# Performance work log

Measured on AMD Instinct MI355X. Metric: run time of the kernel, lower is better.

The kernel has to match this reference:

```python
import jax, jax.numpy as jnp
import numpy as np
import math

B, S, H, NH, DK, K = 256, 200, 768, 12, 64, 64
EPS = 1e-12

def setup_inputs() -> dict:
    key = jax.random.key(0)
    ks = jax.random.split(key, 8)
    sc = 0.02
    return {
        "x": jax.random.normal(ks[0], (B, S, H), dtype=jnp.float32),
        "mask": jnp.ones((B, 1, S), dtype=jnp.float32),
        "Wq": jax.random.normal(ks[1], (H, H), dtype=jnp.float32) * sc,
        "bq": jnp.zeros((H,), dtype=jnp.float32),
        "Wk": jax.random.normal(ks[2], (H, H), dtype=jnp.float32) * sc,
        "bk": jnp.zeros((H,), dtype=jnp.float32),
        "Wv": jax.random.normal(ks[3], (H, H), dtype=jnp.float32) * sc,
        "bv": jnp.zeros((H,), dtype=jnp.float32),
        "We": jax.random.normal(ks[4], (K, S), dtype=jnp.float32) * sc,
        "be": jnp.zeros((K,), dtype=jnp.float32),
        "Wf": jax.random.normal(ks[5], (K, S), dtype=jnp.float32) * sc,
        "bf": jnp.zeros((K,), dtype=jnp.float32),
        "Wd": jax.random.normal(ks[6], (H, H), dtype=jnp.float32) * sc,
        "bd": jnp.zeros((H,), dtype=jnp.float32),
        "gamma": jnp.ones((H,), dtype=jnp.float32),
        "beta": jnp.zeros((H,), dtype=jnp.float32),
    }

def _heads(t):  # [B,S,H] -> [B,NH,S,DK]
    return t.reshape(B, S, NH, DK).transpose(0, 2, 1, 3)

def reference(x, mask, Wq, bq, Wk, bk, Wv, bv, We, be, Wf, bf, Wd, bd, gamma, beta):
    q = _heads(x @ Wq.T + bq)
    k = _heads(x @ Wk.T + bk)
    v = _heads(x @ Wv.T + bv)
    m = mask[:, 0:1, :, None]            # [B,1,S,1]
    k = k * m
    v = v * m
    # Linformer seq projections: E on value, F on key (applied along seq axis)
    v = jnp.einsum("bhsd,ks->bhkd", v, We) + be[:, None]   # [B,NH,K,DK]
    k = jnp.einsum("bhsd,ks->bhkd", k, Wf) + bf[:, None]   # [B,NH,K,DK]
    scores = jnp.einsum("bhqd,bhkd->bhqk", q, k) / math.sqrt(DK)
    p_attn = jax.nn.softmax(scores, axis=-1)               # [B,NH,S,K]
    ctx = jnp.einsum("bhqk,bhkd->bhqd", p_attn, v)         # [B,NH,S,DK]
    ctx = ctx.transpose(0, 2, 1, 3).reshape(B, S, H)
    h = ctx @ Wd.T + bd + x                                # dense + residual (dropout=0)
    mu = jnp.mean(h, axis=-1, keepdims=True)
    var = jnp.mean(jnp.square(h - mu), axis=-1, keepdims=True)
    out = (h - mu) / jnp.sqrt(var + EPS) * gamma + beta
    return out, p_attn
```

## Files before the change

### kernel.cpp

```cpp
#include <hip/hip_runtime.h>
#include <stdint.h>

typedef unsigned short u16;
typedef short bf16x8 __attribute__((ext_vector_type(8)));
typedef float f32x4 __attribute__((ext_vector_type(4)));

#define NB   256
#define NS   200
#define NHID 768
#define NHEAD 12
#define NDK  64
#define NK   64
#define NBH  (NB*NHEAD)
#define NM   (NB*NS)
#define SP   224

__device__ __forceinline__ u16 f2b(float f){
  unsigned u = __builtin_bit_cast(unsigned, f);
  return (u16)((u + 0x7FFFu + ((u>>16)&1u)) >> 16);
}
__device__ __forceinline__ bf16x8 pack8(const float* v){
  bf16x8 r;
#pragma unroll
  for (int i=0;i<8;i++) r[i] = (short)f2b(v[i]);
  return r;
}
__device__ __forceinline__ f32x4 mfma16(bf16x8 a, bf16x8 b, f32x4 c){
  return __builtin_amdgcn_mfma_f32_16x16x32_bf16(a, b, c, 0, 0, 0);
}
__device__ __forceinline__ void gload16(u16* l, const u16* g){
  __builtin_amdgcn_global_load_lds(
      (const __attribute__((address_space(1))) void*)g,
      (__attribute__((address_space(3))) void*)l, 16, 0, 0);
}

__global__ __launch_bounds__(256) void pack_w(
    const float* __restrict__ Wq, const float* __restrict__ Wk,
    const float* __restrict__ Wv, const float* __restrict__ Wd,
    u16* __restrict__ Wqb, u16* __restrict__ Wkb,
    u16* __restrict__ Wvb, u16* __restrict__ Wdb)
{
  const int i = blockIdx.x*256 + threadIdx.x;
  Wqb[i]=f2b(Wq[i]); Wkb[i]=f2b(Wk[i]); Wvb[i]=f2b(Wv[i]); Wdb[i]=f2b(Wd[i]);
}

__global__ __launch_bounds__(256) void pack_wfe(
    const float* __restrict__ Wf, const float* __restrict__ We, u16* __restrict__ Wfeb)
{
  const int r = blockIdx.x, s = threadIdx.x;
  if (s < SP){
    float v = 0.f;
    if (s < NS) v = (r<64) ? Wf[r*NS+s] : We[(r-64)*NS+s];
    Wfeb[r*SP+s] = f2b(v);
  }
}

__global__ __launch_bounds__(128) void rowsums_k(
    const float* __restrict__ Wf, const float* __restrict__ We,
    const float* __restrict__ mask, float* __restrict__ rs)
{
  const int b = blockIdx.x, kk = threadIdx.x;
  const float* src = (kk<64) ? (Wf + kk*NS) : (We + (kk-64)*NS);
  float acc = 0.f;
  for (int s=0;s<NS;s++) acc += src[s]*mask[b*NS+s];
  rs[b*128+kk] = acc;
}

__global__ __launch_bounds__(256) void transpose_x(
    const float* __restrict__ x, const float* __restrict__ mask,
    u16* __restrict__ xb, u16* __restrict__ xbT)
{
  __shared__ u16 LT[64*232];
  const int t = threadIdx.x, b = blockIdx.x, n0 = blockIdx.y*64;
  for (int i=0;i<50;i++){
    const int idx = i*256 + t;
    const int s = idx>>6, n = idx&63;
    const size_t gi = ((size_t)b*NS + s)*NHID + n0 + n;
    const float v = x[gi];
    xb[gi] = f2b(v);
    const float mv = mask[b*NS+s];
    LT[n*232 + s] = f2b(v*mv);
  }
  __syncthreads();
  const int row = t>>2, cb = t&3;
  u16* dst = xbT + (size_t)b*NHID*SP + (size_t)(n0+row)*SP;
  for (int i=0;i<7;i++){
    const int c = cb + i*4;
    bf16x8 vv = (c<25) ? *(const bf16x8*)&LT[row*232 + c*8] : (bf16x8)0;
    *(bf16x8*)&dst[c*8] = vv;
  }
}

__global__ __launch_bounds__(256) void gemm_yfe(
    const u16* __restrict__ Wfeb, const u16* __restrict__ xbT, u16* __restrict__ yfe)
{
  __shared__ u16 Al[128*64];
  __shared__ u16 Bl[128*64];
  const int t=threadIdx.x, w=t>>6, lane=t&63, hi=lane>>4, lo=lane&15;
  const int sr=lane>>3, sc=lane&7;
  const int b=blockIdx.x, col0=blockIdx.y*128;
  const u16* Bg = xbT + (size_t)b*NHID*SP;
  f32x4 acc[4][4];
#pragma unroll
  for(int i=0;i<4;i++)
#pragma unroll
    for(int j=0;j<4;j++) acc[i][j]=(f32x4)0.0f;
  const u16* Ab=&Al[((w>>1)*64+lo)*64 + hi*8];
  const u16* Bb=&Bl[((w&1)*64+lo)*64 + hi*8];

  for (int kt=0; kt<192; kt+=64){
#pragma unroll
    for (int i8=0;i8<4;i8++){
      const int r = w*32 + i8*8 + sr;
      gload16(&Al[r*64 + sc*8], Wfeb + (size_t)r*SP + kt + sc*8);
      gload16(&Bl[r*64 + sc*8], Bg + (size_t)(col0+r)*SP + kt + sc*8);
    }
    asm volatile("s_waitcnt vmcnt(0)" ::: "memory");
    __syncthreads();
#pragma unroll
    for (int ks=0; ks<2; ks++){
      bf16x8 a[4], bfr[4];
#pragma unroll
      for (int i=0;i<4;i++) a[i]   = *(const bf16x8*)(Ab + i*16*64 + ks*32);
#pragma unroll
      for (int j=0;j<4;j++) bfr[j] = *(const bf16x8*)(Bb + j*16*64 + ks*32);
#pragma unroll
      for (int i=0;i<4;i++)
#pragma unroll
        for (int j=0;j<4;j++) acc[i][j] = mfma16(a[i], bfr[j], acc[i][j]);
    }
    __syncthreads();
  }
#pragma unroll
  for (int i8=0;i8<2;i8++){
    const int r2 = w*32 + i8*16 + (lane>>2);
    gload16(&Al[r2*32 + (lane&3)*8], Wfeb + (size_t)r2*SP + 192 + (lane&3)*8);
    gload16(&Bl[r2*32 + (lane&3)*8], Bg + (size_t)(col0+r2)*SP + 192 + (lane&3)*8);
  }
  asm volatile("s_waitcnt vmcnt(0)" ::: "memory");
  __syncthreads();
  {
    bf16x8 a[4], bfr[4];
#pragma unroll
    for (int i=0;i<4;i++) a[i]   = *(const bf16x8*)&Al[((w>>1)*64+i*16+lo)*32 + hi*8];
#pragma unroll
    for (int j=0;j<4;j++) bfr[j] = *(const bf16x8*)&Bl[((w&1)*64+j*16+lo)*32 + hi*8];
#pragma unroll
    for (int i=0;i<4;i++)
#pragma unroll
      for (int j=0;j<4;j++) acc[i][j] = mfma16(a[i], bfr[j], acc[i][j]);
  }
  const int mbase=(w>>1)*64, nbase=col0+(w&1)*64;
#pragma unroll
  for (int i=0;i<4;i++)
#pragma unroll
    for (int r=0;r<4;r++){
      const int m = mbase + i*16 + hi*4 + r;
#pragma unroll
      for (int j=0;j<4;j++){
        const int n = nbase + j*16 + lo;
        yfe[(size_t)b*98304 + (size_t)m*NHID + n] = f2b(acc[i][j][r]);
      }
    }
}

template<int EPI>
__global__ __launch_bounds__(512, 2) void gemm_ring(
    const u16* __restrict__ Ag_, const u16* __restrict__ Bg_,
    const float* __restrict__ bias, const float* __restrict__ resid,
    void* __restrict__ Cout)
{
  __shared__ u16 AS[4][8192];
  __shared__ u16 BS[4][8192];
  const int t = threadIdx.x;
  const int w = t>>6, lane = t&63, hi = lane>>4, lo = lane&15;
  const int wm = w>>2, wn = w&3;
  const int row0 = blockIdx.x*256, col0 = blockIdx.y*256;
  const u16* Ag = Ag_ + (size_t)row0*NHID;
  const u16* Bg = Bg_ + (size_t)col0*NHID;
  const int rp0 = t>>3, cc = t&7;

  f32x4 acc[8][4];
#pragma unroll
  for (int i=0;i<8;i++)
#pragma unroll
    for (int j=0;j<4;j++) acc[i][j] = (f32x4)0.0f;

  int aoff[8], boff[4];
#pragma unroll
  for (int i=0;i<8;i++){
    const int r = wm*128 + i*16 + lo;
    const int rp = r>>1, c = (r&1)*4 + hi;
    aoff[i] = rp*64 + ((c ^ (rp&7))<<3);
  }
#pragma unroll
  for (int j=0;j<4;j++){
    const int n = wn*64 + j*16 + lo;
    const int rp = n>>1, c = (n&1)*4 + hi;
    boff[j] = rp*64 + ((c ^ (rp&7))<<3);
  }

  auto stage = [&](int s, int kt){
#pragma unroll
    for (int i8=0;i8<2;i8++){
      const int rp = i8*64 + rp0;
      const int c  = cc ^ (rp&7);
      const int grow = rp*2 + (c>>2);
      const int gcol = (c&3)<<3;
      gload16(&AS[s][rp*64 + cc*8], Ag + (size_t)grow*NHID + kt + gcol);
      gload16(&BS[s][rp*64 + cc*8], Bg + (size_t)grow*NHID + kt + gcol);
    }
  };
  auto body = [&](const u16* as_, const u16* bs_){
    bf16x8 av[8], bvv[4];
#pragma unroll
    for (int j=0;j<4;j++) bvv[j] = *(const bf16x8*)(bs_ + boff[j]);
#pragma unroll
    for (int i=0;i<8;i++) av[i] = *(const bf16x8*)(as_ + aoff[i]);
    __builtin_amdgcn_s_setprio(1);
#pragma unroll
    for (int i=0;i<8;i++)
#pragma unroll
      for (int j=0;j<4;j++) acc[i][j] = mfma16(av[i], bvv[j], acc[i][j]);
    __builtin_amdgcn_s_setprio(0);
  };
  auto step = [&](int tt, int s){
    if (tt+3 < 24) stage((s+3)&3, (tt+3)*32);
    body(AS[s], BS[s]);
    if (tt <= 20)      { asm volatile("s_waitcnt vmcnt(8)" ::: "memory"); }
    else if (tt == 21) { asm volatile("s_waitcnt vmcnt(4)" ::: "memory"); }
    else if (tt == 22) { asm volatile("s_waitcnt vmcnt(0)" ::: "memory"); }
    if (tt < 23){
      __builtin_amdgcn_sched_barrier(0);
      asm volatile("s_barrier" ::: "memory");
      __builtin_amdgcn_sched_barrier(0);
    }
  };

  stage(0,0); stage(1,32); stage(2,64);
  asm volatile("s_waitcnt vmcnt(8)" ::: "memory");
  asm volatile("s_barrier" ::: "memory");
  __builtin_amdgcn_sched_barrier(0);

#pragma unroll
  for (int tt=0; tt<24; tt+=4){
    step(tt,0); step(tt+1,1); step(tt+2,2); step(tt+3,3);
  }

#pragma unroll
  for (int i=0;i<8;i++)
#pragma unroll
    for (int q=0;q<4;q++){
      const int m = row0 + wm*128 + i*16 + hi*4 + q;
#pragma unroll
      for (int j=0;j<4;j++){
        const int n = col0 + wn*64 + j*16 + lo;
        const float v = acc[i][j][q] + bias[n];
        if constexpr (EPI==0){
          const int b = m/NS, s = m - b*NS;
          ((u16*)Cout)[(((size_t)b*NHEAD + (n>>6))*NS + s)*NDK + (n&63)] = f2b(v);
        } else {
          const size_t gi = (size_t)m*NHID + n;
          ((float*)Cout)[gi] = v + resid[gi];
        }
      }
    }
}

__global__ __launch_bounds__(256) void gemm_kproj(
    const u16* __restrict__ yfe, const u16* __restrict__ Wkb,
    const float* __restrict__ rs, const float* __restrict__ bk,
    const float* __restrict__ bff, u16* __restrict__ kproj)
{
  __shared__ u16 Al[64*64];
  __shared__ u16 Bl[128*64];
  const int t=threadIdx.x, w=t>>6, lane=t&63, hi=lane>>4, lo=lane&15;
  const int sr=lane>>3, sc=lane&7;
  const int b=blockIdx.x, col0=blockIdx.y*128;
  const u16* yf = yfe + (size_t)b*98304;
  f32x4 acc[2][4];
#pragma unroll
  for(int i=0;i<2;i++)
#pragma unroll
    for(int j=0;j<4;j++) acc[i][j]=(f32x4)0.0f;
  const u16* Ab=&Al[((w>>1)*32+lo)*64 + hi*8];
  const u16* Bb=&Bl[((w&1)*64+lo)*64 + hi*8];

  for (int kt=0; kt<NHID; kt+=64){
#pragma unroll
    for (int i8=0;i8<2;i8++){
      const int r = w*16 + i8*8 + sr;
      gload16(&Al[r*64 + sc*8], yf + (size_t)r*NHID + kt + sc*8);
    }
#pragma unroll
    for (int i8=0;i8<4;i8++){
      const int r = w*32 + i8*8 + sr;
      gload16(&Bl[r*64 + sc*8], Wkb + (size_t)(col0+r)*NHID + kt + sc*8);
    }
    asm volatile("s_waitcnt vmcnt(0)" ::: "memory");
    __syncthreads();
#pragma unroll
    for (int ks=0; ks<2; ks++){
      bf16x8 a[2], bfr[4];
#pragma unroll
      for (int i=0;i<2;i++) a[i]   = *(const bf16x8*)(Ab + i*16*64 + ks*32);
#pragma unroll
      for (int j=0;j<4;j++) bfr[j] = *(const bf16x8*)(Bb + j*16*64 + ks*32);
#pragma unroll
      for (int i=0;i<2;i++)
#pragma unroll
        for (int j=0;j<4;j++) acc[i][j] = mfma16(a[i], bfr[j], acc[i][j]);
    }
    __syncthreads();
  }
  const int mbase=(w>>1)*32, nbase=col0+(w&1)*64;
#pragma unroll
  for (int i=0;i<2;i++)
#pragma unroll
    for (int r=0;r<4;r++){
      const int m = mbase + i*16 + hi*4 + r;
      const float rsv = rs[b*128 + m], bfv = bff[m];
#pragma unroll
      for (int j=0;j<4;j++){
        const int n = nbase + j*16 + lo;
        kproj[(size_t)b*49152 + (size_t)m*NHID + n] = f2b(acc[i][j][r] + rsv*bk[n] + bfv);
      }
    }
}

__global__ __launch_bounds__(256) void gemm_vprojT(
    const u16* yfe, const u16* __restrict__ Wvb,
    const float* __restrict__ rs, const float* __restrict__ bv,
    const float* __restrict__ bee, u16* vout)
{
  __shared__ u16 Al[128*64];
  __shared__ u16 Bl[64*64];
  const int t=threadIdx.x, w=t>>6, lane=t&63, hi=lane>>4, lo=lane&15;
  const int sr=lane>>3, sc=lane&7;
  const int b=blockIdx.x, row0=blockIdx.y*128;
  const u16* ye = yfe + (size_t)b*98304 + 49152;
  f32x4 acc[4][2];
#pragma unroll
  for(int i=0;i<4;i++)
#pragma unroll
    for(int j=0;j<2;j++) acc[i][j]=(f32x4)0.0f;
  const u16* Ab=&Al[((w>>1)*64+lo)*64 + hi*8];
  const u16* Bb=&Bl[((w&1)*32+lo)*64 + hi*8];

  for (int kt=0; kt<NHID; kt+=64){
#pragma unroll
    for (int i8=0;i8<4;i8++){
      const int r = w*32 + i8*8 + sr;
      gload16(&Al[r*64 + sc*8], Wvb + (size_t)(row0+r)*NHID + kt + sc*8);
    }
#pragma unroll
    for (int i8=0;i8<2;i8++){
      const int r = w*16 + i8*8 + sr;
      gload16(&Bl[r*64 + sc*8], ye + (size_t)r*NHID + kt + sc*8);
    }
    asm volatile("s_waitcnt vmcnt(0)" ::: "memory");
    __syncthreads();
#pragma unroll
    for (int ks=0; ks<2; ks++){
      bf16x8 a[4], bfr[2];
#pragma unroll
      for (int i=0;i<4;i++) a[i]   = *(const bf16x8*)(Ab + i*16*64 + ks*32);
#pragma unroll
      for (int j=0;j<2;j++) bfr[j] = *(const bf16x8*)(Bb + j*16*64 + ks*32);
#pragma unroll
      for (int i=0;i<4;i++)
#pragma unroll
        for (int j=0;j<2;j++) acc[i][j] = mfma16(a[i], bfr[j], acc[i][j]);
    }
    __syncthreads();
  }
  const int mbase=row0+(w>>1)*64, nbase=(w&1)*32;
#pragma unroll
  for (int i=0;i<4;i++)
#pragma unroll
    for (int r=0;r<4;r++){
      const int m = mbase + i*16 + hi*4 + r;
      const float bvv = bv[m];
#pragma unroll
      for (int j=0;j<2;j++){
        const int n = nbase + j*16 + lo;
        vout[(size_t)b*98304 + (size_t)m*64 + n] = f2b(acc[i][j][r] + rs[b*128+64+n]*bvv + bee[n]);
      }
    }
}

__global__ __launch_bounds__(256) void attn_kernel(
    const u16* __restrict__ qb,
    const u16* __restrict__ kproj,
    const u16* __restrict__ vprojT,
    float* __restrict__ pout,
    u16* __restrict__ ctxb)
{
  __shared__ u16 QL[208*72];
  __shared__ u16 KP[64*72];
  __shared__ u16 VP[64*72];
  const int t=threadIdx.x, w=t>>6, lane=t&63, hi=lane>>4, lo=lane&15;
  const int bh = blockIdx.x, b=bh/NHEAD, hh=bh%NHEAD;
  for (int c=t;c<1600;c+=256){
    const int row=c>>3, col8=(c&7)*8;
    *(bf16x8*)&QL[row*72+col8] = *(const bf16x8*)(qb + (size_t)bh*12800 + c*8);
  }
  if (t<72){ const int row=200+t/9, col8=(t%9)*8; *(bf16x8*)&QL[row*72+col8]=(bf16x8)0; }
  for (int c=t;c<512;c+=256){
    const int row=c>>3, col8=(c&7)*8;
    *(bf16x8*)&KP[row*72+col8] = *(const bf16x8*)(kproj  + (size_t)b*49152 + (size_t)row*NHID + hh*64 + col8);
    *(bf16x8*)&VP[row*72+col8] = *(const bf16x8*)(vprojT + (size_t)b*98304 + (size_t)(hh*64+row)*64 + col8);
  }
  __syncthreads();
  const int mf0 = (w==0)?0:(1+w*3);
  const int nmf = (w==0)?4:3;
  f32x4 acc[4][4];
#pragma unroll
  for(int i=0;i<4;i++)
#pragma unroll
    for(int j=0;j<4;j++) acc[i][j]=(f32x4)0.0f;
#pragma unroll
  for (int ks=0; ks<2; ks++){
    bf16x8 a[4], bb[4];
#pragma unroll
    for (int j=0;j<4;j++) bb[j]=*(const bf16x8*)&KP[(j*16+lo)*72 + ks*32 + hi*8];
#pragma unroll
    for (int i=0;i<4;i++) if (i<nmf) a[i]=*(const bf16x8*)&QL[((mf0+i)*16+lo)*72 + ks*32 + hi*8];
#pragma unroll
    for (int i=0;i<4;i++) if (i<nmf)
#pragma unroll
      for (int j=0;j<4;j++)
        acc[i][j]=mfma16(a[i],bb[j],acc[i][j]);
  }
  __syncthreads();

#pragma unroll
  for (int i=0;i<4;i++) if (i<nmf){
#pragma unroll
    for (int r=0;r<4;r++){
      const int q = (mf0+i)*16 + hi*4 + r;
      float s0=acc[i][0][r]*0.125f, s1=acc[i][1][r]*0.125f,
            s2=acc[i][2][r]*0.125f, s3=acc[i][3][r]*0.125f;
      float mx=fmaxf(fmaxf(s0,s1),fmaxf(s2,s3));
      mx=fmaxf(mx,__shfl_xor(mx,1)); mx=fmaxf(mx,__shfl_xor(mx,2));
      mx=fmaxf(mx,__shfl_xor(mx,4)); mx=fmaxf(mx,__shfl_xor(mx,8));
      float e0=__expf(s0-mx), e1=__expf(s1-mx), e2=__expf(s2-mx), e3=__expf(s3-mx);
      float sm=e0+e1+e2+e3;
      sm+=__shfl_xor(sm,1); sm+=__shfl_xor(sm,2); sm+=__shfl_xor(sm,4); sm+=__shfl_xor(sm,8);
      const float inv=1.0f/sm;
      const float p0=e0*inv,p1=e1*inv,p2=e2*inv,p3=e3*inv;
      if (q<NS){
        float* pg = pout + ((size_t)bh*NS + q)*NK + lo;
        pg[0]=p0; pg[16]=p1; pg[32]=p2; pg[48]=p3;
      }
      u16* pl = &QL[q*72 + lo];
      pl[0]=f2b(p0); pl[16]=f2b(p1); pl[32]=f2b(p2); pl[48]=f2b(p3);
    }
  }
  f32x4 acc2[4][4];
#pragma unroll
  for(int i=0;i<4;i++)
#pragma unroll
    for(int j=0;j<4;j++) acc2[i][j]=(f32x4)0.0f;
#pragma unroll
  for (int ks=0; ks<2; ks++){
    bf16x8 a[4], bb[4];
#pragma unroll
    for (int j=0;j<4;j++) bb[j]=*(const bf16x8*)&VP[(j*16+lo)*72 + ks*32 + hi*8];
#pragma unroll
    for (int i=0;i<4;i++) if (i<nmf) a[i]=*(const bf16x8*)&QL[((mf0+i)*16+lo)*72 + ks*32 + hi*8];
#pragma unroll
    for (int i=0;i<4;i++) if (i<nmf)
#pragma unroll
      for (int j=0;j<4;j++)
        acc2[i][j]=mfma16(a[i],bb[j],acc2[i][j]);
  }
#pragma unroll
  for (int i=0;i<4;i++) if (i<nmf)
#pragma unroll
    for (int r=0;r<4;r++){
      const int q=(mf0+i)*16+hi*4+r;
      if (q<NS){
#pragma unroll
        for (int j=0;j<4;j++){
          const int d=j*16+lo;
          ctxb[((size_t)b*NS+q)*NHID + hh*NDK + d] = f2b(acc2[i][j][r]);
        }
      }
    }
}

__global__ __launch_bounds__(192) void ln_kernel(
    float* __restrict__ out, const float* __restrict__ gamma, const float* __restrict__ beta)
{
  __shared__ float ps[3], pq[3];
  const int t = threadIdx.x;
  float4* row = (float4*)(out + (size_t)blockIdx.x*NHID);
  float4 v = row[t];
  float s = v.x+v.y+v.z+v.w;
  float q = v.x*v.x + v.y*v.y + v.z*v.z + v.w*v.w;
#pragma unroll
  for (int m=1;m<64;m<<=1){ s += __shfl_xor(s,m); q += __shfl_xor(q,m); }
  if ((t&63)==0){ ps[t>>6]=s; pq[t>>6]=q; }
  __syncthreads();
  s = ps[0]+ps[1]+ps[2]; q = pq[0]+pq[1]+pq[2];
  const float mu = s*(1.0f/768.0f);
  const float var = q*(1.0f/768.0f) - mu*mu;
  const float rs = rsqrtf(var + 1e-12f);
  const float4 g  = ((const float4*)gamma)[t];
  const float4 be = ((const float4*)beta)[t];
  float4 o;
  o.x=(v.x-mu)*rs*g.x+be.x; o.y=(v.y-mu)*rs*g.y+be.y;
  o.z=(v.z-mu)*rs*g.z+be.z; o.w=(v.w-mu)*rs*g.w+be.w;
  row[t]=o;
}

extern "C" void kernel_launch(void* const* d_in, const int* in_sizes, int n_in,
                              void* d_out, int out_size, void* d_ws, size_t ws_size,
                              hipStream_t stream)
{
  (void)in_sizes; (void)n_in; (void)out_size; (void)ws_size;
  const float* x    = (const float*)d_in[0];
  const float* mask = (const float*)d_in[1];
  const float* Wq   = (const float*)d_in[2];
  const float* bq   = (const float*)d_in[3];
  const float* Wk   = (const float*)d_in[4];
  const float* bk   = (const float*)d_in[5];
  const float* Wv   = (const float*)d_in[6];
  const float* bv   = (const float*)d_in[7];
  const float* We   = (const float*)d_in[8];
  const float* be   = (const float*)d_in[9];
  const float* Wf   = (const float*)d_in[10];
  const float* bf   = (const float*)d_in[11];
  const float* Wd   = (const float*)d_in[12];
  const float* bd   = (const float*)d_in[13];
  const float* gamma= (const float*)d_in[14];
  const float* beta = (const float*)d_in[15];

  float* out  = (float*)d_out;
  float* pout = out + (size_t)NM*NHID;

  char* ws = (char*)d_ws;
  u16* xb    = (u16*)(ws);
  u16* ctxb  = (u16*)(ws);
  u16* xbT   = (u16*)(ws + 78643200ull);
  u16* qb    = (u16*)(ws + 78643200ull);
  u16* yfe   = (u16*)(ws + 166723584ull);
  u16* vprojT= (u16*)(ws + 166723584ull);
  u16* kproj = (u16*)(ws + 217055232ull);
  u16* Wqb   = (u16*)(ws + 242221056ull);
  u16* Wkb   = (u16*)(ws + 243400704ull);
  u16* Wvb   = (u16*)(ws + 244580352ull);
  u16* Wdb   = (u16*)(ws + 245760000ull);
  u16* Wfeb  = (u16*)(ws + 246939648ull);
  float* rsb = (float*)(ws + 246996992ull);

  pack_w  <<<2304,256,0,stream>>>(Wq,Wk,Wv,Wd,Wqb,Wkb,Wvb,Wdb);
  pack_wfe<<<128, 256,0,stream>>>(Wf,We,Wfeb);
  rowsums_k<<<NB, 128,0,stream>>>(Wf,We,mask,rsb);
  transpose_x<<<dim3(NB,12),256,0,stream>>>(x,mask,xb,xbT);
  gemm_yfe<<<dim3(NB,6),256,0,stream>>>(Wfeb,xbT,yfe);
  gemm_ring<0><<<dim3(200,3),512,0,stream>>>(xb,Wqb,bq,nullptr,qb);
  gemm_kproj <<<dim3(NB,6),256,0,stream>>>(yfe,Wkb,rsb,bk,bf,kproj);
  gemm_vprojT<<<dim3(NB,6),256,0,stream>>>(yfe,Wvb,rsb,bv,be,vprojT);
  attn_kernel<<<NBH,256,0,stream>>>(qb,kproj,vprojT,pout,ctxb);
  gemm_ring<1><<<dim3(200,3),512,0,stream>>>(ctxb,Wdb,bd,x,out);
  ln_kernel<<<NM,192,0,stream>>>(out,gamma,beta);
}
```

Measured before the change: 588.5 us.

## Fuse dense output projection, residual add and LayerNorm into one kernel

Replaces the dense GEMM with residual epilogue plus the separate LayerNorm kernel with a single kernel. Each block computes a full 64-row by 768-column tile so it can reduce row statistics in registers and shared memory and write normalized output directly. This removes the fp32 write and re-read of the intermediate hidden state and one launch. In exchange it uses a simpler single-buffered K loop with a large shared-memory B tile (768x72), which likely lowers occupancy and loses the pipelined ring schedule of the previous GEMM.

```diff
diff --git a/kernel.cpp b/kernel.cpp
--- a/kernel.cpp
+++ b/kernel.cpp
@@ -18,12 +18,6 @@
 __device__ __forceinline__ u16 f2b(float f){
   unsigned u = __builtin_bit_cast(unsigned, f);
   return (u16)((u + 0x7FFFu + ((u>>16)&1u)) >> 16);
-}
-__device__ __forceinline__ bf16x8 pack8(const float* v){
-  bf16x8 r;
-#pragma unroll
-  for (int i=0;i<8;i++) r[i] = (short)f2b(v[i]);
-  return r;
 }
 __device__ __forceinline__ f32x4 mfma16(bf16x8 a, bf16x8 b, f32x4 c){
   return __builtin_amdgcn_mfma_f32_16x16x32_bf16(a, b, c, 0, 0, 0);
@@ -164,11 +158,9 @@
     }
 }
 
-template<int EPI>
 __global__ __launch_bounds__(512, 2) void gemm_ring(
     const u16* __restrict__ Ag_, const u16* __restrict__ Bg_,
-    const float* __restrict__ bias, const float* __restrict__ resid,
-    void* __restrict__ Cout)
+    const float* __restrict__ bias, u16* __restrict__ Cout)
 {
   __shared__ u16 AS[4][8192];
   __shared__ u16 BS[4][8192];
@@ -252,17 +244,126 @@
 #pragma unroll
     for (int q=0;q<4;q++){
       const int m = row0 + wm*128 + i*16 + hi*4 + q;
+      const int b = m/NS, s = m - b*NS;
 #pragma unroll
       for (int j=0;j<4;j++){
         const int n = col0 + wn*64 + j*16 + lo;
         const float v = acc[i][j][q] + bias[n];
-        if constexpr (EPI==0){
-          const int b = m/NS, s = m - b*NS;
-          ((u16*)Cout)[(((size_t)b*NHEAD + (n>>6))*NS + s)*NDK + (n&63)] = f2b(v);
-        } else {
-          const size_t gi = (size_t)m*NHID + n;
-          ((float*)Cout)[gi] = v + resid[gi];
-        }
+        Cout[(((size_t)b*NHEAD + (n>>6))*NS + s)*NDK + (n&63)] = f2b(v);
+      }
+    }
+}
+
+__global__ __launch_bounds__(512, 2) void gemm_ln(
+    const u16* __restrict__ ctxb, const u16* __restrict__ Wdb,
+    const float* __restrict__ bd, const float* __restrict__ x,
+    const float* __restrict__ gamma, const float* __restrict__ beta,
+    float* __restrict__ outp)
+{
+  __shared__ u16 Bl[768*72];
+  __shared__ u16 Al[64*72];
+  __shared__ float SS[64][8], SQ[64][8];
+  __shared__ float MU[64], RS[64];
+  const int t=threadIdx.x, w=t>>6, lane=t&63, hi=lane>>4, lo=lane&15;
+  const int row0 = blockIdx.x*64;
+  const u16* Actx = ctxb + (size_t)row0*NHID;
+
+  const int nB = (w<4)?14:13;
+  const int nA = (w==0)?2:1;
+  int offB[14], dstB[14], offA[2], dstA[2];
+#pragma unroll
+  for (int s=0;s<14;s++){
+    const int j = w + 8*s;
+    const int c = j*64 + lane;
+    const int row = c/9, cc9 = c%9;
+    offB[s] = row*NHID + ((cc9==8)?0:cc9*8);
+    dstB[s] = j*512 + lane*8;
+  }
+#pragma unroll
+  for (int s=0;s<2;s++){
+    const int j = (s==0)? w : 8;
+    const int c = j*64 + lane;
+    const int row = c/9, cc9 = c%9;
+    offA[s] = row*NHID + ((cc9==8)?0:cc9*8);
+    dstA[s] = j*512 + lane*8;
+  }
+
+  f32x4 acc[4][6];
+#pragma unroll
+  for (int i=0;i<4;i++)
+#pragma unroll
+    for (int j=0;j<6;j++) acc[i][j] = (f32x4)0.0f;
+
+  for (int kt=0; kt<NHID; kt+=64){
+#pragma unroll
+    for (int s=0;s<14;s++) if (s<nB) gload16(&Bl[dstB[s]], Wdb + offB[s] + kt);
+#pragma unroll
+    for (int s=0;s<2;s++)  if (s<nA) gload16(&Al[dstA[s]], Actx + offA[s] + kt);
+    __syncthreads();
+#pragma unroll
+    for (int ks=0; ks<2; ks++){
+      bf16x8 av[4], bv[6];
+#pragma unroll
+      for (int i=0;i<4;i++) av[i] = *(const bf16x8*)&Al[(i*16+lo)*72 + ks*32 + hi*8];
+#pragma unroll
+      for (int j=0;j<6;j++) bv[j] = *(const bf16x8*)&Bl[(w*96+j*16+lo)*72 + ks*32 + hi*8];
+      __builtin_amdgcn_s_setprio(1);
+#pragma unroll
+      for (int i=0;i<4;i++)
+#pragma unroll
+        for (int j=0;j<6;j++) acc[i][j] = mfma16(av[i], bv[j], acc[i][j]);
+      __builtin_amdgcn_s_setprio(0);
+    }
+    __syncthreads();
+  }
+
+  float g_[6], be_[6], bd_[6];
+#pragma unroll
+  for (int j=0;j<6;j++){
+    const int n = w*96 + j*16 + lo;
+    g_[j]=gamma[n]; be_[j]=beta[n]; bd_[j]=bd[n];
+  }
+#pragma unroll
+  for (int i=0;i<4;i++)
+#pragma unroll
+    for (int q=0;q<4;q++){
+      const int rloc = i*16 + hi*4 + q;
+      const size_t m = row0 + rloc;
+      float ps=0.f, pq2=0.f;
+#pragma unroll
+      for (int j=0;j<6;j++){
+        const int n = w*96 + j*16 + lo;
+        const float h = acc[i][j][q] + bd_[j] + x[m*NHID + n];
+        acc[i][j][q] = h;
+        ps += h; pq2 += h*h;
+      }
+      ps += __shfl_xor(ps,1); pq2 += __shfl_xor(pq2,1);
+      ps += __shfl_xor(ps,2); pq2 += __shfl_xor(pq2,2);
+      ps += __shfl_xor(ps,4); pq2 += __shfl_xor(pq2,4);
+      ps += __shfl_xor(ps,8); pq2 += __shfl_xor(pq2,8);
+      if (lo==0){ SS[rloc][w]=ps; SQ[rloc][w]=pq2; }
+    }
+  __syncthreads();
+  if (t<64){
+    float s=0.f, q2=0.f;
+#pragma unroll
+    for (int ww=0;ww<8;ww++){ s+=SS[t][ww]; q2+=SQ[t][ww]; }
+    const float mu = s*(1.0f/768.0f);
+    const float var = q2*(1.0f/768.0f) - mu*mu;
+    MU[t]=mu; RS[t]=rsqrtf(var + 1e-12f);
+  }
+  __syncthreads();
+#pragma unroll
+  for (int i=0;i<4;i++)
+#pragma unroll
+    for (int q=0;q<4;q++){
+      const int rloc = i*16 + hi*4 + q;
+      const float mu = MU[rloc], rr = RS[rloc];
+      const size_t m = row0 + rloc;
+#pragma unroll
+      for (int j=0;j<6;j++){
+        const int n = w*96 + j*16 + lo;
+        outp[m*NHID + n] = (acc[i][j][q]-mu)*rr*g_[j] + be_[j];
       }
     }
 }
@@ -488,31 +589,6 @@
         }
       }
     }
-}
-
-__global__ __launch_bounds__(192) void ln_kernel(
-    float* __restrict__ out, const float* __restrict__ gamma, const float* __restrict__ beta)
-{
-  __shared__ float ps[3], pq[3];
-  const int t = threadIdx.x;
-  float4* row = (float4*)(out + (size_t)blockIdx.x*NHID);
-  float4 v = row[t];
-  float s = v.x+v.y+v.z+v.w;
-  float q = v.x*v.x + v.y*v.y + v.z*v.z + v.w*v.w;
-#pragma unroll
-  for (int m=1;m<64;m<<=1){ s += __shfl_xor(s,m); q += __shfl_xor(q,m); }
-  if ((t&63)==0){ ps[t>>6]=s; pq[t>>6]=q; }
-  __syncthreads();
-  s = ps[0]+ps[1]+ps[2]; q = pq[0]+pq[1]+pq[2];
-  const float mu = s*(1.0f/768.0f);
-  const float var = q*(1.0f/768.0f) - mu*mu;
-  const float rs = rsqrtf(var + 1e-12f);
-  const float4 g  = ((const float4*)gamma)[t];
-  const float4 be = ((const float4*)beta)[t];
-  float4 o;
-  o.x=(v.x-mu)*rs*g.x+be.x; o.y=(v.y-mu)*rs*g.y+be.y;
-  o.z=(v.z-mu)*rs*g.z+be.z; o.w=(v.w-mu)*rs*g.w+be.w;
-  row[t]=o;
 }
 
 extern "C" void kernel_launch(void* const* d_in, const int* in_sizes, int n_in,
@@ -560,10 +636,9 @@
   rowsums_k<<<NB, 128,0,stream>>>(Wf,We,mask,rsb);
   transpose_x<<<dim3(NB,12),256,0,stream>>>(x,mask,xb,xbT);
   gemm_yfe<<<dim3(NB,6),256,0,stream>>>(Wfeb,xbT,yfe);
-  gemm_ring<0><<<dim3(200,3),512,0,stream>>>(xb,Wqb,bq,nullptr,qb);
+  gemm_ring<<<dim3(200,3),512,0,stream>>>(xb,Wqb,bq,qb);
   gemm_kproj <<<dim3(NB,6),256,0,stream>>>(yfe,Wkb,rsb,bk,bf,kproj);
   gemm_vprojT<<<dim3(NB,6),256,0,stream>>>(yfe,Wvb,rsb,bv,be,vprojT);
   attn_kernel<<<NBH,256,0,stream>>>(qb,kproj,vprojT,pout,ctxb);
-  gemm_ring<1><<<dim3(200,3),512,0,stream>>>(ctxb,Wdb,bd,x,out);
-  ln_kernel<<<NM,192,0,stream>>>(out,gamma,beta);
-}
+  gemm_ln<<<800,512,0,stream>>>(ctxb,Wdb,bd,x,gamma,beta,out);
+}
```

Result: slower. 602.3 us (+2.4%).
